# Optimization experiments

Hardware: AMD Instinct MI355X
Metric: run time of the kernel (lower is better)

Reference implementation:

```python
import jax, jax.numpy as jnp
import numpy as np

N = 100000      # nodes
E = 1250000     # edges
D = 64          # hidden_units == dim_node_features
DE = 7          # edge feature dim (OGBG-PPA)
L = 5           # num_layers
G = 128         # graphs in batch
T = 37          # classes


def setup_inputs() -> dict:
    key = jax.random.key(0)
    ks = jax.random.split(key, 12)
    x = jax.random.normal(ks[0], (N, D), dtype=jnp.float32)
    edge_index = jax.random.randint(ks[1], (2, E), 0, N, dtype=jnp.int64)
    edge_attr = jax.random.uniform(ks[2], (E, DE), dtype=jnp.float32)
    batch = jnp.sort(jax.random.randint(ks[3], (N,), 0, G, dtype=jnp.int64))
    s_e = 1.0 / np.sqrt(DE)
    s_d = 1.0 / np.sqrt(D)
    s_p = 1.0 / np.sqrt(L * D)
    W_edge = jax.random.normal(ks[4], (DE, D), dtype=jnp.float32) * s_e  # shared edge encoder
    b_edge = jnp.zeros((D,), jnp.float32)
    W_mlp = jax.random.normal(ks[5], (L, D, D), dtype=jnp.float32) * s_d  # per-layer MLP
    b_mlp = jnp.zeros((L, D), jnp.float32)
    eps = jnp.zeros((L,), jnp.float32)  # torch.Tensor([0]) per layer
    W_pred = jax.random.normal(ks[6], (L * D, T), dtype=jnp.float32) * s_p
    b_pred = jnp.zeros((T,), jnp.float32)
    return {"x": x, "edge_index": edge_index, "edge_attr": edge_attr, "batch": batch,
            "W_edge": W_edge, "b_edge": b_edge, "eps": eps,
            "W_mlp": W_mlp, "b_mlp": b_mlp, "W_pred": W_pred, "b_pred": b_pred}


def reference(x, edge_index, edge_attr, batch, W_edge, b_edge, eps, W_mlp, b_mlp, W_pred, b_pred):
    src, dst = edge_index[0], edge_index[1]  # PyG source_to_target: x_j = x[src], aggregate at dst
    # shared edge encoder -> identical output every layer; compute once
    edge_emb = edge_attr @ W_edge + b_edge  # [E, D]
    h = x
    outs = []
    for i in range(L):
        msg = jax.nn.relu(h[src] + edge_emb)                      # gather + fuse  [E, D]
        agg = jax.ops.segment_sum(msg, dst, num_segments=N)       # scatter-add    [N, D]
        h = jax.nn.relu(((1.0 + eps[i]) * h + agg) @ W_mlp[i] + b_mlp[i])
        outs.append(h)
    node_emb = jnp.concatenate(outs, axis=1)                      # [N, L*D]
    # predictor: per-graph mean pool + linear readout
    g_sum = jax.ops.segment_sum(node_emb, batch, num_segments=G)  # [G, L*D]
    cnt = jax.ops.segment_sum(jnp.ones((N, 1), node_emb.dtype), batch, num_segments=G)
    g = g_sum / jnp.maximum(cnt, 1.0)
    return g @ W_pred + b_pred                                    # [G, T]
```

## Files before the change

### kernel.cpp

```cpp
#include <hip/hip_runtime.h>
#include <hip/hip_bf16.h>

#define DD   64
#define NL   5
#define NT   37
#define LD   (NL*DD)
#define PB   16
#define NBMAX 512

typedef __attribute__((ext_vector_type(8))) short short8;
typedef __attribute__((ext_vector_type(4))) float f32x4;
typedef __attribute__((ext_vector_type(4))) int   i32x4;
typedef __attribute__((ext_vector_type(2))) int   i32x2;

static __device__ __forceinline__ int padq(int d) { return (d + PB - 1) & ~(PB - 1); }
static __device__ __forceinline__ short bf16_bits(float f) {
    __hip_bfloat16 h = __float2bfloat16(f);
    return __builtin_bit_cast(short, h);
}
static __device__ __forceinline__ float bf2f(short s) {
    return __int_as_float(((int)(unsigned short)s) << 16);
}

__global__ void init_kernel(const float* __restrict__ x, __hip_bfloat16* __restrict__ hb,
                            size_t n1, const float* __restrict__ W,
                            __hip_bfloat16* __restrict__ Wt, int n2,
                            const int* __restrict__ dst, int* __restrict__ deg, int E,
                            int do_deg) {
    size_t i = (size_t)blockIdx.x * blockDim.x + threadIdx.x;
    if (i < n1) {
        hb[i] = __float2bfloat16(x[i]);
    } else if (i < n1 + (size_t)n2) {
        size_t id = i - n1;
        int l = (int)(id / (DD * DD));
        int r = (int)(id % (DD * DD));
        int c = r / DD, k = r % DD;
        Wt[(size_t)l * DD * DD + c * DD + k] =
            __float2bfloat16(W[(size_t)l * DD * DD + k * DD + c]);
    } else if (do_deg) {
        size_t e = i - n1 - (size_t)n2;
        if (e < (size_t)E) atomicAdd(&deg[dst[e]], 1);
    }
}

__global__ void bhist_kernel(const int* __restrict__ dst, int* __restrict__ bcnt, int E) {
    __shared__ int h[NBMAX];
    int tid = threadIdx.x;
    h[tid] = 0; h[tid + 256] = 0;
    __syncthreads();
    int base = blockIdx.x * 4096;
#pragma unroll
    for (int j = 0; j < 16; ++j) {
        int e = base + j * 256 + tid;
        if (e < E) atomicAdd(&h[dst[e] >> 8], 1);
    }
    __syncthreads();
    int c0 = h[tid], c1 = h[tid + 256];
    if (c0) atomicAdd(&bcnt[tid], c0);
    if (c1) atomicAdd(&bcnt[tid + 256], c1);
}

__global__ void bscan_kernel(const int* __restrict__ bcnt, int* __restrict__ boff,
                             int* __restrict__ bcur) {
    __shared__ int sm[256];
    int tid = threadIdx.x;
    int v0 = bcnt[2 * tid], v1 = bcnt[2 * tid + 1];
    int s = v0 + v1;
    sm[tid] = s;
    __syncthreads();
    for (int off = 1; off < 256; off <<= 1) {
        int t = (tid >= off) ? sm[tid - off] : 0;
        __syncthreads();
        sm[tid] += t;
        __syncthreads();
    }
    int p = sm[tid] - s;
    boff[2 * tid] = p;     bcur[2 * tid] = p;     p += v0;
    boff[2 * tid + 1] = p; bcur[2 * tid + 1] = p; p += v1;
    if (tid == 255) boff[512] = p;
}

__global__ void pscat_kernel(const int* __restrict__ dst, int* __restrict__ bcur,
                             i32x2* __restrict__ stage, int E) {
    __shared__ int h[NBMAX];
    __shared__ int runb[NBMAX];
    int tid = threadIdx.x;
    h[tid] = 0; h[tid + 256] = 0;
    __syncthreads();
    int base = blockIdx.x * 4096;
    int d[16];
#pragma unroll
    for (int j = 0; j < 16; ++j) {
        int e = base + j * 256 + tid;
        d[j] = (e < E) ? dst[e] : -1;
        if (d[j] >= 0) atomicAdd(&h[d[j] >> 8], 1);
    }
    __syncthreads();
    int c0 = h[tid], c1 = h[tid + 256];
    runb[tid]       = c0 ? atomicAdd(&bcur[tid], c0) : 0;
    runb[tid + 256] = c1 ? atomicAdd(&bcur[tid + 256], c1) : 0;
    __syncthreads();
    h[tid] = 0; h[tid + 256] = 0;
    __syncthreads();
#pragma unroll
    for (int j = 0; j < 16; ++j) {
        if (d[j] >= 0) {
            int b = d[j] >> 8;
            int r = atomicAdd(&h[b], 1);
            i32x2 pr; pr[0] = base + j * 256 + tid; pr[1] = d[j];
            stage[runb[b] + r] = pr;
        }
    }
}

__global__ void bdeg_kernel(const i32x2* __restrict__ stage, const int* __restrict__ boff,
                            int* __restrict__ deg, int n) {
    __shared__ int cnt[256];
    int tid = threadIdx.x;
    int b = blockIdx.x;
    cnt[tid] = 0;
    __syncthreads();
    int s = boff[b], e = boff[b + 1];
    for (int j = s + tid; j < e; j += 256)
        atomicAdd(&cnt[stage[j][1] & 255], 1);
    __syncthreads();
    int node = b * 256 + tid;
    if (node < n) deg[node] = cnt[tid];
}

template<bool PACKED>
__global__ void place_kernel(const i32x2* __restrict__ stage, const int* __restrict__ boff,
                             const int* __restrict__ rowptr, const int* __restrict__ src,
                             const float* __restrict__ ea,
                             short* __restrict__ eab, int* __restrict__ srcv,
                             int* __restrict__ col, int n) {
    __shared__ int cur[256];
    int tid = threadIdx.x;
    int b = blockIdx.x;
    int node = b * 256 + tid;
    cur[tid] = (node < n) ? rowptr[node] : 0;
    __syncthreads();
    int s = boff[b], e = boff[b + 1];
    for (int j = s + tid; j < e; j += 256) {
        i32x2 pr = stage[j];
        int eid = pr[0], d = pr[1];
        int slot = atomicAdd(&cur[d & 255], 1);
        srcv[slot] = src[eid];
        if (PACKED) {
            const float* a = ea + (size_t)eid * 7;
            short8 r;
#pragma unroll
            for (int k = 0; k < 7; ++k) r[k] = bf16_bits(a[k]);
            r[7] = 0;
            *((i32x4*)(eab + (size_t)slot * 8)) = __builtin_bit_cast(i32x4, r);
        } else {
            col[slot] = eid;
        }
    }
    __syncthreads();
    if (node < n) {
        int endp = rowptr[node + 1];
        for (int i = cur[tid]; i < endp; ++i) {
            srcv[i] = 0;
            if (PACKED) {
                i32x4 z = {0, 0, 0, 0};
                *((i32x4*)(eab + (size_t)i * 8)) = z;
            } else {
                col[i] = 0;
            }
        }
    }
}

__global__ void chunksum_kernel(const int* __restrict__ deg, int* __restrict__ csum, int n) {
    __shared__ int sm[256];
    int tid = threadIdx.x;
    int base = blockIdx.x * 1024 + tid * 4;
    int s = 0;
#pragma unroll
    for (int j = 0; j < 4; ++j) s += (base + j < n) ? padq(deg[base + j]) : 0;
    sm[tid] = s;
    __syncthreads();
    for (int off = 128; off > 0; off >>= 1) {
        if (tid < off) sm[tid] += sm[tid + off];
        __syncthreads();
    }
    if (tid == 0) csum[blockIdx.x] = sm[0];
}

__global__ void scansums_kernel(int* __restrict__ csum, int nc, int* __restrict__ tot) {
    __shared__ int sm[256];
    int tid = threadIdx.x;
    int base = tid * 4;
    int v[4]; int s = 0;
#pragma unroll
    for (int j = 0; j < 4; ++j) { v[j] = (base + j < nc) ? csum[base + j] : 0; s += v[j]; }
    sm[tid] = s;
    __syncthreads();
    for (int off = 1; off < 256; off <<= 1) {
        int t = (tid >= off) ? sm[tid - off] : 0;
        __syncthreads();
        sm[tid] += t;
        __syncthreads();
    }
    int p = sm[tid] - s;
#pragma unroll
    for (int j = 0; j < 4; ++j) { if (base + j < nc) csum[base + j] = p; p += v[j]; }
    if (tid == 255) *tot = p;
}

__global__ void chunkscan_kernel(const int* __restrict__ deg, const int* __restrict__ csum,
                                 int* __restrict__ rowptr, int* __restrict__ cursor, int n) {
    __shared__ int sm[256];
    int tid = threadIdx.x;
    int base = blockIdx.x * 1024 + tid * 4;
    int v[4]; int s = 0;
#pragma unroll
    for (int j = 0; j < 4; ++j) { v[j] = (base + j < n) ? padq(deg[base + j]) : 0; s += v[j]; }
    sm[tid] = s;
    __syncthreads();
    for (int off = 1; off < 256; off <<= 1) {
        int t = (tid >= off) ? sm[tid - off] : 0;
        __syncthreads();
        sm[tid] += t;
        __syncthreads();
    }
    int p = sm[tid] - s + csum[blockIdx.x];
#pragma unroll
    for (int j = 0; j < 4; ++j) {
        if (base + j < n) { rowptr[base + j] = p; cursor[base + j] = p; }
        p += v[j];
    }
}

__global__ void fillpos_kernel(const int* __restrict__ dst, int* __restrict__ cursor,
                               int* __restrict__ col, int E) {
    int e = blockIdx.x * blockDim.x + threadIdx.x;
    if (e >= E) return;
    int p = atomicAdd(&cursor[dst[e]], 1);
    col[p] = e;
}

__global__ void padmark_kernel(const int* __restrict__ deg, const int* __restrict__ rowptr,
                               int* __restrict__ col, int n) {
    int v = blockIdx.x * blockDim.x + threadIdx.x;
    if (v >= n) return;
    int s = rowptr[v] + deg[v];
    int e = rowptr[v + 1];
    for (int i = s; i < e; ++i) col[i] = -1;
}

template<bool PACKED>
__global__ void gfill_kernel(const int* __restrict__ col, const int* __restrict__ src,
                             const float* __restrict__ ea, const int* __restrict__ rowptrN,
                             short* __restrict__ eab, int* __restrict__ srcv,
                             int* __restrict__ colw) {
    int slot = blockIdx.x * blockDim.x + threadIdx.x;
    if (slot >= *rowptrN) return;
    int e = col[slot];
    int s = 0;
    short8 r;
#pragma unroll
    for (int k = 0; k < 8; ++k) r[k] = 0;
    if (e >= 0) {
        s = src[e];
        if (PACKED) {
            const float* a = ea + (size_t)e * 7;
#pragma unroll
            for (int k = 0; k < 7; ++k) r[k] = bf16_bits(a[k]);
        }
    } else if (!PACKED) {
        colw[slot] = 0;
    }
    __builtin_nontemporal_store(s, &srcv[slot]);
    if (PACKED) {
        i32x4 ri = __builtin_bit_cast(i32x4, r);
        __builtin_nontemporal_store(ri, (i32x4*)(eab + (size_t)slot * 8));
    }
}

template<bool PACKED>
__global__ void fill_kernel(const int* __restrict__ dst, const int* __restrict__ src,
                            const float* __restrict__ ea, int* __restrict__ cursor,
                            short* __restrict__ eab, int* __restrict__ col,
                            int* __restrict__ srcv, int E) {
    int e = blockIdx.x * blockDim.x + threadIdx.x;
    if (e >= E) return;
    int p = atomicAdd(&cursor[dst[e]], 1);
    int s = src[e];
    __builtin_nontemporal_store(s, &srcv[p]);
    if (PACKED) {
        const float* a = ea + (size_t)e * 7;
        short8 r;
#pragma unroll
        for (int k = 0; k < 7; ++k) r[k] = bf16_bits(a[k]);
        r[7] = 0;
        i32x4 ri = __builtin_bit_cast(i32x4, r);
        __builtin_nontemporal_store(ri, (i32x4*)(eab + (size_t)p * 8));
    } else {
        __builtin_nontemporal_store(e, &col[p]);
    }
}

__global__ void padfill_kernel(const int* __restrict__ deg, const int* __restrict__ rowptr,
                               int* __restrict__ srcv, int* __restrict__ col,
                               int has_col, int n) {
    int v = blockIdx.x * blockDim.x + threadIdx.x;
    if (v >= n) return;
    int s = rowptr[v] + deg[v];
    int e = rowptr[v + 1];
    for (int i = s; i < e; ++i) {
        srcv[i] = 0;
        if (has_col) col[i] = 0;
    }
}

template<bool PACKED>
static __device__ __forceinline__ float row_partial(
    const __hip_bfloat16* __restrict__ hb_in, const short* __restrict__ eab,
    const int* __restrict__ col, const float* __restrict__ ea,
    const int* __restrict__ srcv, int beg, int dv, int lane,
    const float* __restrict__ we, float be) {
    float acc = 0.f;
    int end = beg + dv;
    for (int p = beg; p < end; p += PB) {
        int mm = end - p;
        int S[PB];
#pragma unroll
        for (int j = 0; j < PB; ++j) S[j] = srcv[p + j];
        __hip_bfloat16 hv[PB];
#pragma unroll
        for (int j = 0; j < PB; ++j) hv[j] = hb_in[(size_t)S[j] * DD + lane];
        float ev[PB][7];
        if (PACKED) {
            short8 eb[PB];
#pragma unroll
            for (int j = 0; j < PB; ++j)
                eb[j] = *((const short8*)(eab + (size_t)(p + j) * 8));
#pragma unroll
            for (int j = 0; j < PB; ++j)
#pragma unroll
                for (int k = 0; k < 7; ++k) ev[j][k] = bf2f(eb[j][k]);
        } else {
            int EJ[PB];
#pragma unroll
            for (int j = 0; j < PB; ++j) EJ[j] = col[p + j];
#pragma unroll
            for (int j = 0; j < PB; ++j) {
                const float* a = ea + (size_t)EJ[j] * 7;
#pragma unroll
                for (int k = 0; k < 7; ++k) ev[j][k] = a[k];
            }
        }
#pragma unroll
        for (int j = 0; j < PB; ++j) {
            if (j < mm) {
                float emb = be + ev[j][0] * we[0] + ev[j][1] * we[1] + ev[j][2] * we[2]
                               + ev[j][3] * we[3] + ev[j][4] * we[4] + ev[j][5] * we[5]
                               + ev[j][6] * we[6];
                float tv = __bfloat162float(hv[j]) + emb;
                acc += (tv > 0.f) ? tv : 0.f;
            }
        }
    }
    return acc;
}

template<bool PACKED>
static __device__ __forceinline__ void agg_pair(
    const __hip_bfloat16* __restrict__ hb_in, const short* __restrict__ eab,
    const int* __restrict__ col, const float* __restrict__ ea,
    const int* __restrict__ srcv, int beg0, int d0, int beg1, int d1, bool has1,
    int lane, const float* __restrict__ we, float be, float& acc0, float& acc1) {
    acc0 = 0.f; acc1 = 0.f;
    if (has1 && d0 >= 1 && d0 <= PB && d1 >= 1 && d1 <= PB) {
        int S0[PB], S1[PB];
#pragma unroll
        for (int j = 0; j < PB; ++j) S0[j] = srcv[beg0 + j];
#pragma unroll
        for (int j = 0; j < PB; ++j) S1[j] = srcv[beg1 + j];
        __hip_bfloat16 hv0[PB], hv1[PB];
#pragma unroll
        for (int j = 0; j < PB; ++j) hv0[j] = hb_in[(size_t)S0[j] * DD + lane];
#pragma unroll
        for (int j = 0; j < PB; ++j) hv1[j] = hb_in[(size_t)S1[j] * DD + lane];
        float ev0[PB][7], ev1[PB][7];
        if (PACKED) {
            short8 eb0[PB], eb1[PB];
#pragma unroll
            for (int j = 0; j < PB; ++j)
                eb0[j] = *((const short8*)(eab + (size_t)(beg0 + j) * 8));
#pragma unroll
            for (int j = 0; j < PB; ++j)
                eb1[j] = *((const short8*)(eab + (size_t)(beg1 + j) * 8));
#pragma unroll
            for (int j = 0; j < PB; ++j)
#pragma unroll
                for (int k = 0; k < 7; ++k) ev0[j][k] = bf2f(eb0[j][k]);
#pragma unroll
            for (int j = 0; j < PB; ++j)
#pragma unroll
                for (int k = 0; k < 7; ++k) ev1[j][k] = bf2f(eb1[j][k]);
        } else {
            int EJ0[PB], EJ1[PB];
#pragma unroll
            for (int j = 0; j < PB; ++j) EJ0[j] = col[beg0 + j];
#pragma unroll
            for (int j = 0; j < PB; ++j) EJ1[j] = col[beg1 + j];
#pragma unroll
            for (int j = 0; j < PB; ++j) {
                const float* a = ea + (size_t)EJ0[j] * 7;
#pragma unroll
                for (int k = 0; k < 7; ++k) ev0[j][k] = a[k];
            }
#pragma unroll
            for (int j = 0; j < PB; ++j) {
                const float* a = ea + (size_t)EJ1[j] * 7;
#pragma unroll
                for (int k = 0; k < 7; ++k) ev1[j][k] = a[k];
            }
        }
#pragma unroll
        for (int j = 0; j < PB; ++j) {
            if (j < d0) {
                float emb = be + ev0[j][0] * we[0] + ev0[j][1] * we[1] + ev0[j][2] * we[2]
                               + ev0[j][3] * we[3] + ev0[j][4] * we[4] + ev0[j][5] * we[5]
                               + ev0[j][6] * we[6];
                float tv = __bfloat162float(hv0[j]) + emb;
                acc0 += (tv > 0.f) ? tv : 0.f;
            }
        }
#pragma unroll
        for (int j = 0; j < PB; ++j) {
            if (j < d1) {
                float emb = be + ev1[j][0] * we[0] + ev1[j][1] * we[1] + ev1[j][2] * we[2]
                               + ev1[j][3] * we[3] + ev1[j][4] * we[4] + ev1[j][5] * we[5]
                               + ev1[j][6] * we[6];
                float tv = __bfloat162float(hv1[j]) + emb;
                acc1 += (tv > 0.f) ? tv : 0.f;
            }
        }
    } else {
        acc0 = row_partial<PACKED>(hb_in, eab, col, ea, srcv, beg0, d0, lane, we, be);
        if (has1)
            acc1 = row_partial<PACKED>(hb_in, eab, col, ea, srcv, beg1, d1, lane, we, be);
    }
}

__global__ __launch_bounds__(256, 4)
void aggmlp_kernel(const __hip_bfloat16* __restrict__ hb_in,
                   const short* __restrict__ eab, const int* __restrict__ srcv,
                   const int* __restrict__ rowptr, const int* __restrict__ deg,
                   const float* __restrict__ W_edge, const float* __restrict__ b_edge,
                   const float* __restrict__ eps, int layer,
                   const __hip_bfloat16* __restrict__ Wt, const float* __restrict__ bmlp,
                   __hip_bfloat16* __restrict__ hb_out, int n) {
    __shared__ __align__(16) short uls[16][72];
    int tid = threadIdx.x;
    int lane = tid & 63;
    int wv = __builtin_amdgcn_readfirstlane(tid >> 6);
    int base = blockIdx.x * 16;

    float we[7];
#pragma unroll
    for (int k = 0; k < 7; ++k) we[k] = W_edge[k * DD + lane];
    float be = b_edge[lane];
    float epsv = 1.f + eps[layer];

#pragma unroll
    for (int pp = 0; pp < 2; ++pp) {
        int v0 = base + wv * 4 + pp * 2;
        bool h0 = v0 < n, h1 = (v0 + 1) < n;
        int beg0 = h0 ? rowptr[v0] : 0;
        int d0   = h0 ? deg[v0] : 0;
        int beg1 = h1 ? rowptr[v0 + 1] : 0;
        int d1   = h1 ? deg[v0 + 1] : 0;
        float acc0, acc1;
        agg_pair<true>(hb_in, eab, nullptr, nullptr, srcv,
                       beg0, d0, beg1, d1, h1, lane, we, be, acc0, acc1);
        if (h0) {
            float self = __bfloat162float(hb_in[(size_t)v0 * DD + lane]);
            uls[wv * 4 + pp * 2][lane] = bf16_bits(epsv * self + acc0);
        }
        if (h1) {
            float self = __bfloat162float(hb_in[(size_t)(v0 + 1) * DD + lane]);
            uls[wv * 4 + pp * 2 + 1][lane] = bf16_bits(epsv * self + acc1);
        }
    }
    __syncthreads();

    if (wv == 0) {
        int colx = lane & 15;
        int quad = lane >> 4;
        short8 wf[4][2];
#pragma unroll
        for (int t = 0; t < 4; ++t)
#pragma unroll
            for (int s = 0; s < 2; ++s)
                wf[t][s] = *((const short8*)(Wt + (size_t)(t * 16 + colx) * DD + s * 32 + quad * 8));
        float bias[4];
#pragma unroll
        for (int t = 0; t < 4; ++t) bias[t] = bmlp[t * 16 + colx];

        short8 a0 = *((const short8*)&uls[colx][quad * 8]);
        short8 a1 = *((const short8*)&uls[colx][32 + quad * 8]);

        f32x4 acc[4] = {{0.f, 0.f, 0.f, 0.f}, {0.f, 0.f, 0.f, 0.f},
                        {0.f, 0.f, 0.f, 0.f}, {0.f, 0.f, 0.f, 0.f}};
#pragma unroll
        for (int t = 0; t < 4; ++t) {
            acc[t] = __builtin_amdgcn_mfma_f32_16x16x32_bf16(a0, wf[t][0], acc[t], 0, 0, 0);
            acc[t] = __builtin_amdgcn_mfma_f32_16x16x32_bf16(a1, wf[t][1], acc[t], 0, 0, 0);
        }
#pragma unroll
        for (int r = 0; r < 4; ++r) {
            int v = base + quad * 4 + r;
            if (v < n) {
#pragma unroll
                for (int t = 0; t < 4; ++t) {
                    float val = acc[t][r] + bias[t];
                    val = (val > 0.f) ? val : 0.f;
                    hb_out[(size_t)v * DD + t * 16 + colx] = __float2bfloat16(val);
                }
            }
        }
    }
}

template<bool PACKED>
__global__ __launch_bounds__(256, 4)
void agg_kernel(const __hip_bfloat16* __restrict__ hb_in,
                const short* __restrict__ eab,
                const int* __restrict__ col, const int* __restrict__ srcv,
                const float* __restrict__ ea,
                const int* __restrict__ rowptr, const int* __restrict__ deg,
                const float* __restrict__ W_edge, const float* __restrict__ b_edge,
                const float* __restrict__ eps, int layer,
                __hip_bfloat16* __restrict__ u, int n) {
    int lane = threadIdx.x & 63;
    int wid = __builtin_amdgcn_readfirstlane(blockIdx.x * 4 + (threadIdx.x >> 6));
    int v0 = wid * 2;
    if (v0 >= n) return;

    float we[7];
#pragma unroll
    for (int k = 0; k < 7; ++k) we[k] = W_edge[k * DD + lane];
    float be = b_edge[lane];
    float epsv = 1.f + eps[layer];

    int beg0 = rowptr[v0];
    int d0   = deg[v0];
    bool has1 = (v0 + 1) < n;
    int beg1 = has1 ? rowptr[v0 + 1] : 0;
    int d1   = has1 ? deg[v0 + 1] : 0;

    float acc0, acc1;
    agg_pair<PACKED>(hb_in, eab, col, ea, srcv, beg0, d0, beg1, d1, has1,
                     lane, we, be, acc0, acc1);

    float self0 = __bfloat162float(hb_in[(size_t)v0 * DD + lane]);
    u[(size_t)v0 * DD + lane] = __float2bfloat16(epsv * self0 + acc0);
    if (has1) {
        float self1 = __bfloat162float(hb_in[(size_t)(v0 + 1) * DD + lane]);
        u[(size_t)(v0 + 1) * DD + lane] = __float2bfloat16(epsv * self1 + acc1);
    }
}

__global__ __launch_bounds__(256, 4)
void mlp_mfma_kernel(const __hip_bfloat16* __restrict__ u,
                     const __hip_bfloat16* __restrict__ Wt,
                     const float* __restrict__ bmlp,
                     __hip_bfloat16* __restrict__ hb_out, int n) {
    int lane = threadIdx.x & 63;
    int wid  = threadIdx.x >> 6;
    int colx = lane & 15;
    int quad = lane >> 4;
    int v0 = __builtin_amdgcn_readfirstlane((blockIdx.x * 4 + wid) * 16);
    if (v0 >= n) return;

    short8 wf[4][2];
#pragma unroll
    for (int t = 0; t < 4; ++t)
#pragma unroll
        for (int s = 0; s < 2; ++s)
            wf[t][s] = *((const short8*)(Wt + (size_t)(t * 16 + colx) * DD + s * 32 + quad * 8));
    float bias[4];
#pragma unroll
    for (int t = 0; t < 4; ++t) bias[t] = bmlp[t * 16 + colx];

    int vr = v0 + colx;
    int vrc = (vr < n) ? vr : (n - 1);
    const __hip_bfloat16* up = u + (size_t)vrc * DD;
    short8 a0 = *((const short8*)(up + quad * 8));
    short8 a1 = *((const short8*)(up + 32 + quad * 8));

    f32x4 acc[4] = {{0.f, 0.f, 0.f, 0.f}, {0.f, 0.f, 0.f, 0.f},
                    {0.f, 0.f, 0.f, 0.f}, {0.f, 0.f, 0.f, 0.f}};
#pragma unroll
    for (int t = 0; t < 4; ++t) {
        acc[t] = __builtin_amdgcn_mfma_f32_16x16x32_bf16(a0, wf[t][0], acc[t], 0, 0, 0);
        acc[t] = __builtin_amdgcn_mfma_f32_16x16x32_bf16(a1, wf[t][1], acc[t], 0, 0, 0);
    }

#pragma unroll
    for (int r = 0; r < 4; ++r) {
        int v = v0 + quad * 4 + r;
        if (v < n) {
#pragma unroll
            for (int t = 0; t < 4; ++t) {
                float val = acc[t][r] + bias[t];
                val = (val > 0.f) ? val : 0.f;
                hb_out[(size_t)v * DD + t * 16 + colx] = __float2bfloat16(val);
            }
        }
    }
}

__global__ void pool_part_kernel(const __hip_bfloat16* __restrict__ htabs, size_t lstride,
                                 const int* __restrict__ batch,
                                 float* __restrict__ g_sum, int n, int G) {
    __shared__ float part[4][DD];
    __shared__ int bnd[2];
    int g = blockIdx.x / NL;
    int q = blockIdx.x % NL;
    int tid = threadIdx.x;
    if (tid < 2) {
        int target = g + tid;
        int lo = 0, hi = n;
        while (lo < hi) { int mid = (lo + hi) >> 1; if (batch[mid] < target) lo = mid + 1; else hi = mid; }
        bnd[tid] = lo;
    }
    __syncthreads();
    int lb = bnd[0], ub = bnd[1];
    int w = tid >> 6, f = tid & 63;
    const __hip_bfloat16* T = htabs + (size_t)q * lstride;
    float s = 0.f;
    for (int v = lb + w; v < ub; v += 4)
        s += __bfloat162float(T[(size_t)v * DD + f]);
    part[w][f] = s;
    __syncthreads();
    if (tid < DD) {
        float tot = part[0][f] + part[1][f] + part[2][f] + part[3][f];
        float c = (float)(ub - lb);
        if (c < 1.f) c = 1.f;
        g_sum[(size_t)g * LD + q * DD + f] = tot / c;
    }
}

__global__ void readout_mean_kernel(const float* __restrict__ g_mean,
                                    const float* __restrict__ W_pred,
                                    const float* __restrict__ b_pred,
                                    float* __restrict__ out, int G) {
    int id = blockIdx.x * blockDim.x + threadIdx.x;
    if (id >= G * NT) return;
    int g = id / NT, t = id % NT;
    float acc = b_pred[t];
    const float* gs = g_mean + (size_t)g * LD;
    for (int k = 0; k < LD; ++k) acc += gs[k] * W_pred[k * NT + t];
    out[id] = acc;
}

__global__ void pool_kernel(const __hip_bfloat16* __restrict__ h, const int* __restrict__ batch,
                            float* __restrict__ g_sum, int layer, int n) {
    int wave = (blockIdx.x * blockDim.x + threadIdx.x) >> 6;
    int l = threadIdx.x & 63;
    int v0 = wave * 64;
    if (v0 >= n) return;
    int vend = min(v0 + 64, n);
    int cur = batch[v0];
    float acc = 0.f;
    for (int v = v0; v < vend; ++v) {
        int bv = batch[v];
        if (bv != cur) {
            atomicAdd(&g_sum[(size_t)cur * LD + layer * DD + l], acc);
            acc = 0.f;
            cur = bv;
        }
        acc += __bfloat162float(h[(size_t)v * DD + l]);
    }
    atomicAdd(&g_sum[(size_t)cur * LD + layer * DD + l], acc);
}

__global__ void graph_cnt_kernel(const int* __restrict__ batch, int* __restrict__ cnt,
                                 int n, int G) {
    int g = blockIdx.x * blockDim.x + threadIdx.x;
    if (g >= G) return;
    int lo = 0, hi = n;
    while (lo < hi) { int mid = (lo + hi) >> 1; if (batch[mid] < g) lo = mid + 1; else hi = mid; }
    int lb0 = lo;
    lo = lb0; hi = n;
    while (lo < hi) { int mid = (lo + hi) >> 1; if (batch[mid] < g + 1) lo = mid + 1; else hi = mid; }
    cnt[g] = lo - lb0;
}

__global__ void readout_kernel(const float* __restrict__ g_sum, const int* __restrict__ cnt,
                               const float* __restrict__ W_pred, const float* __restrict__ b_pred,
                               float* __restrict__ out, int G) {
    int id = blockIdx.x * blockDim.x + threadIdx.x;
    if (id >= G * NT) return;
    int g = id / NT, t = id % NT;
    float c = (float)cnt[g];
    if (c < 1.f) c = 1.f;
    float inv = 1.f / c;
    float acc = b_pred[t];
    const float* gs = g_sum + (size_t)g * LD;
    for (int k = 0; k < LD; ++k) acc += gs[k] * inv * W_pred[k * NT + t];
    out[id] = acc;
}

extern "C" void kernel_launch(void* const* d_in, const int* in_sizes, int n_in,
                              void* d_out, int out_size, void* d_ws, size_t ws_size,
                              hipStream_t stream) {
    const float* x       = (const float*)d_in[0];
    const int*   eidx    = (const int*)d_in[1];
    const float* ea      = (const float*)d_in[2];
    const int*   batch   = (const int*)d_in[3];
    const float* W_edge  = (const float*)d_in[4];
    const float* b_edge  = (const float*)d_in[5];
    const float* eps     = (const float*)d_in[6];
    const float* W_mlp   = (const float*)d_in[7];
    const float* b_mlp   = (const float*)d_in[8];
    const float* W_pred  = (const float*)d_in[9];
    const float* b_pred  = (const float*)d_in[10];
    float* out = (float*)d_out;

    const int N = in_sizes[3];
    const int E = in_sizes[2] / 7;
    const int G = out_size / NT;
    const int* src = eidx;
    const int* dst = eidx + E;
    const int NC = (N + 1023) / 1024;
    const int NB = (N + 255) >> 8;
    const size_t SLOTS = (size_t)E + (size_t)(PB - 1) * N;

    const size_t S_h = (size_t)N * DD * 2;
    const size_t small = (size_t)N * 4 + (size_t)(N + 4) * 4 + (size_t)N * 4 + 4096
                       + 8192
                       + (size_t)NL * DD * DD * 2
                       + (size_t)G * LD * 4 + (((size_t)G * 4 + 15) & ~(size_t)15);
    const size_t needA = 7 * S_h + small + SLOTS * 20;
    const size_t needB = 7 * S_h + small + SLOTS * 8;
    const int tier = (ws_size >= needA) ? 0 : (ws_size >= needB) ? 1 : 2;
    const int nTab = (tier <= 1) ? 6 : 2;

    char* w = (char*)d_ws;
    __hip_bfloat16* hbt = (__hip_bfloat16*)w;  w += (size_t)nTab * S_h;
    __hip_bfloat16* u   = (__hip_bfloat16*)w;  w += S_h;
    __hip_bfloat16* Wt  = (__hip_bfloat16*)w;  w += (size_t)NL * DD * DD * 2;
    int*   deg    = (int*)w;                   w += (size_t)N * 4;
    int*   rowptr = (int*)w;                   w += (size_t)(N + 4) * 4;
    int*   cursor = (int*)w;                   w += (size_t)N * 4;
    int*   csum   = (int*)w;                   w += 4096;
    int*   bcnt   = (int*)w;                   w += 2048;
    int*   boff   = (int*)w;                   w += 2064;
    int*   bcur   = (int*)w;                   w += 2048;
    float* g_sum  = (float*)w;                 w += (size_t)G * LD * 4;
    int*   cnt    = (int*)w;                   w += ((size_t)G * 4 + 15) & ~(size_t)15;
    short* eab = nullptr; int* col = nullptr; int* srcv = nullptr;
    if (tier == 0) {
        eab  = (short*)w;  w += SLOTS * 16;
        srcv = (int*)w;
    } else {
        col  = (int*)w;    w += SLOTS * 4;
        srcv = (int*)w;
    }
    const bool packed = (tier == 0);

    const bool newcsr = (NB <= NBMAX) && ((size_t)E * 8 <= S_h);
    i32x2* stage = (i32x2*)u;

    if (tier == 2) hipMemsetAsync(g_sum, 0, (size_t)G * LD * 4, stream);

    {
        size_t n1 = (size_t)N * DD;
        size_t tot = n1 + (size_t)(NL * DD * DD) + (newcsr ? 0 : (size_t)E);
        if (!newcsr) hipMemsetAsync(deg, 0, (size_t)N * 4, stream);
        init_kernel<<<(unsigned)((tot + 255) / 256), 256, 0, stream>>>(
            x, hbt, n1, W_mlp, Wt, NL * DD * DD, dst, deg, E, newcsr ? 0 : 1);
    }

    if (newcsr) {
        hipMemsetAsync(bcnt, 0, NBMAX * 4, stream);
        unsigned eb4 = (unsigned)((E + 4095) / 4096);
        bhist_kernel<<<eb4, 256, 0, stream>>>(dst, bcnt, E);
        bscan_kernel<<<1, 256, 0, stream>>>(bcnt, boff, bcur);
        pscat_kernel<<<eb4, 256, 0, stream>>>(dst, bcur, stage, E);
        bdeg_kernel<<<NB, 256, 0, stream>>>(stage, boff, deg, N);
        chunksum_kernel<<<NC, 256, 0, stream>>>(deg, csum, N);
        scansums_kernel<<<1, 256, 0, stream>>>(csum, NC, rowptr + N);
        chunkscan_kernel<<<NC, 256, 0, stream>>>(deg, csum, rowptr, cursor, N);
        if (packed)
            place_kernel<true><<<NB, 256, 0, stream>>>(stage, boff, rowptr, src, ea,
                                                       eab, srcv, col, N);
        else
            place_kernel<false><<<NB, 256, 0, stream>>>(stage, boff, rowptr, src, ea,
                                                        eab, srcv, col, N);
    } else {
        chunksum_kernel<<<NC, 256, 0, stream>>>(deg, csum, N);
        scansums_kernel<<<1, 256, 0, stream>>>(csum, NC, rowptr + N);
        chunkscan_kernel<<<NC, 256, 0, stream>>>(deg, csum, rowptr, cursor, N);
        int* colbuf = nullptr;
        if (tier == 0) {
            if (SLOTS * 4 <= S_h) colbuf = (int*)u;
        } else {
            colbuf = col;
        }
        if (colbuf) {
            fillpos_kernel<<<(E + 255) / 256, 256, 0, stream>>>(dst, cursor, colbuf, E);
            padmark_kernel<<<(N + 255) / 256, 256, 0, stream>>>(deg, rowptr, colbuf, N);
            unsigned gblocks = (unsigned)((SLOTS + 255) / 256);
            if (packed)
                gfill_kernel<true><<<gblocks, 256, 0, stream>>>(colbuf, src, ea, rowptr + N,
                                                                eab, srcv, colbuf);
            else
                gfill_kernel<false><<<gblocks, 256, 0, stream>>>(colbuf, src, ea, rowptr + N,
                                                                 eab, srcv, colbuf);
        } else {
            if (packed)
                fill_kernel<true><<<(E + 255) / 256, 256, 0, stream>>>(dst, src, ea, cursor,
                                                                       eab, col, srcv, E);
            else
                fill_kernel<false><<<(E + 255) / 256, 256, 0, stream>>>(dst, src, ea, cursor,
                                                                        eab, col, srcv, E);
            padfill_kernel<<<(N + 255) / 256, 256, 0, stream>>>(deg, rowptr, srcv,
                                                                col ? col : srcv,
                                                                col ? 1 : 0, N);
        }
    }

    const bool useFused = newcsr && packed;
    int fusedBlocks = (N + 15) / 16;
    int aggBlocks = (N + 7) / 8;
    int mlpBlocks = (N + 63) / 64;
    for (int i = 0; i < NL; ++i) {
        __hip_bfloat16* hin  = (tier <= 1) ? (hbt + (size_t)i * N * DD)
                                           : (hbt + (size_t)(i & 1) * N * DD);
        __hip_bfloat16* hout = (tier <= 1) ? (hbt + (size_t)(i + 1) * N * DD)
                                           : (hbt + (size_t)((i + 1) & 1) * N * DD);
        if (useFused) {
            aggmlp_kernel<<<fusedBlocks, 256, 0, stream>>>(
                hin, eab, srcv, rowptr, deg, W_edge, b_edge, eps, i,
                Wt + (size_t)i * DD * DD, b_mlp + (size_t)i * DD, hout, N);
        } else {
            if (packed)
                agg_kernel<true><<<aggBlocks, 256, 0, stream>>>(
                    hin, eab, col, srcv, ea, rowptr, deg, W_edge, b_edge, eps, i, u, N);
            else
                agg_kernel<false><<<aggBlocks, 256, 0, stream>>>(
                    hin, eab, col, srcv, ea, rowptr, deg, W_edge, b_edge, eps, i, u, N);
            mlp_mfma_kernel<<<mlpBlocks, 256, 0, stream>>>(
                u, Wt + (size_t)i * DD * DD, b_mlp + (size_t)i * DD, hout, N);
        }
        if (tier == 2)
            pool_kernel<<<((N + 63) / 64 * 64 + 255) / 256, 256, 0, stream>>>(hout, batch,
                                                                              g_sum, i, N);
    }

    if (tier <= 1) {
        pool_part_kernel<<<G * NL, 256, 0, stream>>>(hbt + (size_t)N * DD, (size_t)N * DD,
                                                     batch, g_sum, N, G);
        readout_mean_kernel<<<(G * NT + 255) / 256, 256, 0, stream>>>(g_sum, W_pred, b_pred,
                                                                      out, G);
    } else {
        graph_cnt_kernel<<<1, 128, 0, stream>>>(batch, cnt, N, G);
        readout_kernel<<<(G * NT + 255) / 256, 256, 0, stream>>>(g_sum, cnt, W_pred, b_pred,
                                                                 out, G);
    }
}
```

Before: 674.6 us.

## Compute edge embeddings with MFMA in fused aggregate-MLP kernel

The fused aggregation kernel now computes the per-edge encoder projection with a bf16 16x16x32 MFMA. It packs edge features with a constant 1.0 in the 8th slot so the bias folds into a padded transposed weight table, built in init_kernel. Each wave processes one node at a time: lanes split into four edge groups and 16 feature columns, then reduce with cross-lane shuffles. This replaces the scalar 7-term FMA per edge per feature. The bcnt memset is folded into init_kernel to save a launch, and the paired-node path is removed, which may reduce memory-level parallelism for gathers.

```diff
diff --git a/kernel.cpp b/kernel.cpp
--- a/kernel.cpp
+++ b/kernel.cpp
@@ -25,6 +25,8 @@
 __global__ void init_kernel(const float* __restrict__ x, __hip_bfloat16* __restrict__ hb,
                             size_t n1, const float* __restrict__ W,
                             __hip_bfloat16* __restrict__ Wt, int n2,
+                            const float* __restrict__ W_edge, const float* __restrict__ b_edge,
+                            __hip_bfloat16* __restrict__ webt, int* __restrict__ bcnt,
                             const int* __restrict__ dst, int* __restrict__ deg, int E,
                             int do_deg) {
     size_t i = (size_t)blockIdx.x * blockDim.x + threadIdx.x;
@@ -37,8 +39,15 @@
         int c = r / DD, k = r % DD;
         Wt[(size_t)l * DD * DD + c * DD + k] =
             __float2bfloat16(W[(size_t)l * DD * DD + k * DD + c]);
+    } else if (i < n1 + (size_t)n2 + 2048) {
+        int id = (int)(i - n1 - (size_t)n2);
+        int f = id >> 5, k = id & 31;
+        float v = (k < 7) ? W_edge[k * DD + f] : (k == 7 ? b_edge[f] : 0.f);
+        webt[id] = __float2bfloat16(v);
+    } else if (i < n1 + (size_t)n2 + 2048 + NBMAX) {
+        bcnt[i - n1 - (size_t)n2 - 2048] = 0;
     } else if (do_deg) {
-        size_t e = i - n1 - (size_t)n2;
+        size_t e = i - n1 - (size_t)n2 - 2048 - NBMAX;
         if (e < (size_t)E) atomicAdd(&deg[dst[e]], 1);
     }
 }
@@ -151,7 +160,7 @@
             short8 r;
 #pragma unroll
             for (int k = 0; k < 7; ++k) r[k] = bf16_bits(a[k]);
-            r[7] = 0;
+            r[7] = (short)0x3F80;
             *((i32x4*)(eab + (size_t)slot * 8)) = __builtin_bit_cast(i32x4, r);
         } else {
             col[slot] = eid;
@@ -268,6 +277,7 @@
             const float* a = ea + (size_t)e * 7;
 #pragma unroll
             for (int k = 0; k < 7; ++k) r[k] = bf16_bits(a[k]);
+            r[7] = (short)0x3F80;
         }
     } else if (!PACKED) {
         colw[slot] = 0;
@@ -294,7 +304,7 @@
         short8 r;
 #pragma unroll
         for (int k = 0; k < 7; ++k) r[k] = bf16_bits(a[k]);
-        r[7] = 0;
+        r[7] = (short)0x3F80;
         i32x4 ri = __builtin_bit_cast(i32x4, r);
         __builtin_nontemporal_store(ri, (i32x4*)(eab + (size_t)p * 8));
     } else {
@@ -372,79 +382,10 @@
     const int* __restrict__ col, const float* __restrict__ ea,
     const int* __restrict__ srcv, int beg0, int d0, int beg1, int d1, bool has1,
     int lane, const float* __restrict__ we, float be, float& acc0, float& acc1) {
-    acc0 = 0.f; acc1 = 0.f;
-    if (has1 && d0 >= 1 && d0 <= PB && d1 >= 1 && d1 <= PB) {
-        int S0[PB], S1[PB];
-#pragma unroll
-        for (int j = 0; j < PB; ++j) S0[j] = srcv[beg0 + j];
-#pragma unroll
-        for (int j = 0; j < PB; ++j) S1[j] = srcv[beg1 + j];
-        __hip_bfloat16 hv0[PB], hv1[PB];
-#pragma unroll
-        for (int j = 0; j < PB; ++j) hv0[j] = hb_in[(size_t)S0[j] * DD + lane];
-#pragma unroll
-        for (int j = 0; j < PB; ++j) hv1[j] = hb_in[(size_t)S1[j] * DD + lane];
-        float ev0[PB][7], ev1[PB][7];
-        if (PACKED) {
-            short8 eb0[PB], eb1[PB];
-#pragma unroll
-            for (int j = 0; j < PB; ++j)
-                eb0[j] = *((const short8*)(eab + (size_t)(beg0 + j) * 8));
-#pragma unroll
-            for (int j = 0; j < PB; ++j)
-                eb1[j] = *((const short8*)(eab + (size_t)(beg1 + j) * 8));
-#pragma unroll
-            for (int j = 0; j < PB; ++j)
-#pragma unroll
-                for (int k = 0; k < 7; ++k) ev0[j][k] = bf2f(eb0[j][k]);
-#pragma unroll
-            for (int j = 0; j < PB; ++j)
-#pragma unroll
-                for (int k = 0; k < 7; ++k) ev1[j][k] = bf2f(eb1[j][k]);
-        } else {
-            int EJ0[PB], EJ1[PB];
-#pragma unroll
-            for (int j = 0; j < PB; ++j) EJ0[j] = col[beg0 + j];
-#pragma unroll
-            for (int j = 0; j < PB; ++j) EJ1[j] = col[beg1 + j];
-#pragma unroll
-            for (int j = 0; j < PB; ++j) {
-                const float* a = ea + (size_t)EJ0[j] * 7;
-#pragma unroll
-                for (int k = 0; k < 7; ++k) ev0[j][k] = a[k];
-            }
-#pragma unroll
-            for (int j = 0; j < PB; ++j) {
-                const float* a = ea + (size_t)EJ1[j] * 7;
-#pragma unroll
-                for (int k = 0; k < 7; ++k) ev1[j][k] = a[k];
-            }
-        }
-#pragma unroll
-        for (int j = 0; j < PB; ++j) {
-            if (j < d0) {
-                float emb = be + ev0[j][0] * we[0] + ev0[j][1] * we[1] + ev0[j][2] * we[2]
-                               + ev0[j][3] * we[3] + ev0[j][4] * we[4] + ev0[j][5] * we[5]
-                               + ev0[j][6] * we[6];
-                float tv = __bfloat162float(hv0[j]) + emb;
-                acc0 += (tv > 0.f) ? tv : 0.f;
-            }
-        }
-#pragma unroll
-        for (int j = 0; j < PB; ++j) {
-            if (j < d1) {
-                float emb = be + ev1[j][0] * we[0] + ev1[j][1] * we[1] + ev1[j][2] * we[2]
-                               + ev1[j][3] * we[3] + ev1[j][4] * we[4] + ev1[j][5] * we[5]
-                               + ev1[j][6] * we[6];
-                float tv = __bfloat162float(hv1[j]) + emb;
-                acc1 += (tv > 0.f) ? tv : 0.f;
-            }
-        }
-    } else {
-        acc0 = row_partial<PACKED>(hb_in, eab, col, ea, srcv, beg0, d0, lane, we, be);
-        if (has1)
-            acc1 = row_partial<PACKED>(hb_in, eab, col, ea, srcv, beg1, d1, lane, we, be);
-    }
+    acc0 = row_partial<PACKED>(hb_in, eab, col, ea, srcv, beg0, d0, lane, we, be);
+    acc1 = 0.f;
+    if (has1)
+        acc1 = row_partial<PACKED>(hb_in, eab, col, ea, srcv, beg1, d1, lane, we, be);
 }
 
 __global__ __launch_bounds__(256, 4)
@@ -452,14 +393,18 @@
                    const short* __restrict__ eab, const int* __restrict__ srcv,
                    const int* __restrict__ rowptr, const int* __restrict__ deg,
                    const float* __restrict__ W_edge, const float* __restrict__ b_edge,
+                   const __hip_bfloat16* __restrict__ webt,
                    const float* __restrict__ eps, int layer,
                    const __hip_bfloat16* __restrict__ Wt, const float* __restrict__ bmlp,
                    __hip_bfloat16* __restrict__ hb_out, int n) {
     __shared__ __align__(16) short uls[16][72];
+    const unsigned short* hbu = (const unsigned short*)hb_in;
     int tid = threadIdx.x;
     int lane = tid & 63;
     int wv = __builtin_amdgcn_readfirstlane(tid >> 6);
     int base = blockIdx.x * 16;
+    int colx = lane & 15;
+    int q = lane >> 4;
 
     float we[7];
 #pragma unroll
@@ -467,43 +412,77 @@
     float be = b_edge[lane];
     float epsv = 1.f + eps[layer];
 
-#pragma unroll
-    for (int pp = 0; pp < 2; ++pp) {
-        int v0 = base + wv * 4 + pp * 2;
-        bool h0 = v0 < n, h1 = (v0 + 1) < n;
-        int beg0 = h0 ? rowptr[v0] : 0;
-        int d0   = h0 ? deg[v0] : 0;
-        int beg1 = h1 ? rowptr[v0 + 1] : 0;
-        int d1   = h1 ? deg[v0 + 1] : 0;
-        float acc0, acc1;
-        agg_pair<true>(hb_in, eab, nullptr, nullptr, srcv,
-                       beg0, d0, beg1, d1, h1, lane, we, be, acc0, acc1);
-        if (h0) {
-            float self = __bfloat162float(hb_in[(size_t)v0 * DD + lane]);
-            uls[wv * 4 + pp * 2][lane] = bf16_bits(epsv * self + acc0);
-        }
-        if (h1) {
-            float self = __bfloat162float(hb_in[(size_t)(v0 + 1) * DD + lane]);
-            uls[wv * 4 + pp * 2 + 1][lane] = bf16_bits(epsv * self + acc1);
+    short8 wb[4];
+#pragma unroll
+    for (int t = 0; t < 4; ++t)
+        wb[t] = *((const short8*)(webt + (size_t)(t * 16 + colx) * 32 + q * 8));
+
+#pragma unroll
+    for (int nd = 0; nd < 4; ++nd) {
+        int v = base + wv * 4 + nd;
+        if (v < n) {
+            int p = rowptr[v];
+            int d = deg[v];
+            float nodeacc;
+            if (d >= 1 && d <= PB) {
+                short8 a = {0, 0, 0, 0, 0, 0, 0, 0};
+                if (q == 0)
+                    a = *((const short8*)(eab + (size_t)(p + colx) * 8));
+                int sr0 = srcv[p + 4 * q + 0];
+                int sr1 = srcv[p + 4 * q + 1];
+                int sr2 = srcv[p + 4 * q + 2];
+                int sr3 = srcv[p + 4 * q + 3];
+                f32x4 z = {0.f, 0.f, 0.f, 0.f};
+                f32x4 emb[4];
+#pragma unroll
+                for (int t = 0; t < 4; ++t)
+                    emb[t] = __builtin_amdgcn_mfma_f32_16x16x32_bf16(a, wb[t], z, 0, 0, 0);
+                unsigned short hv[4][4];
+#pragma unroll
+                for (int t = 0; t < 4; ++t) {
+                    hv[0][t] = hbu[(size_t)sr0 * DD + t * 16 + colx];
+                    hv[1][t] = hbu[(size_t)sr1 * DD + t * 16 + colx];
+                    hv[2][t] = hbu[(size_t)sr2 * DD + t * 16 + colx];
+                    hv[3][t] = hbu[(size_t)sr3 * DD + t * 16 + colx];
+                }
+                float ts[4];
+#pragma unroll
+                for (int t = 0; t < 4; ++t) {
+                    float s = 0.f;
+#pragma unroll
+                    for (int r = 0; r < 4; ++r) {
+                        float tv = __int_as_float((int)hv[r][t] << 16) + emb[t][r];
+                        float rv = ((4 * q + r) < d) ? ((tv > 0.f) ? tv : 0.f) : 0.f;
+                        s += rv;
+                    }
+                    s += __shfl_xor(s, 16, 64);
+                    s += __shfl_xor(s, 32, 64);
+                    ts[t] = s;
+                }
+                nodeacc = (q == 0) ? ts[0] : (q == 1) ? ts[1] : (q == 2) ? ts[2] : ts[3];
+            } else {
+                nodeacc = row_partial<true>(hb_in, eab, nullptr, nullptr, srcv,
+                                            p, d, lane, we, be);
+            }
+            float self = __int_as_float((int)hbu[(size_t)v * DD + lane] << 16);
+            uls[wv * 4 + nd][lane] = bf16_bits(epsv * self + nodeacc);
         }
     }
     __syncthreads();
 
     if (wv == 0) {
-        int colx = lane & 15;
-        int quad = lane >> 4;
         short8 wf[4][2];
 #pragma unroll
         for (int t = 0; t < 4; ++t)
 #pragma unroll
             for (int s = 0; s < 2; ++s)
-                wf[t][s] = *((const short8*)(Wt + (size_t)(t * 16 + colx) * DD + s * 32 + quad * 8));
+                wf[t][s] = *((const short8*)(Wt + (size_t)(t * 16 + colx) * DD + s * 32 + q * 8));
         float bias[4];
 #pragma unroll
         for (int t = 0; t < 4; ++t) bias[t] = bmlp[t * 16 + colx];
 
-        short8 a0 = *((const short8*)&uls[colx][quad * 8]);
-        short8 a1 = *((const short8*)&uls[colx][32 + quad * 8]);
+        short8 a0 = *((const short8*)&uls[colx][q * 8]);
+        short8 a1 = *((const short8*)&uls[colx][32 + q * 8]);
 
         f32x4 acc[4] = {{0.f, 0.f, 0.f, 0.f}, {0.f, 0.f, 0.f, 0.f},
                         {0.f, 0.f, 0.f, 0.f}, {0.f, 0.f, 0.f, 0.f}};
@@ -514,7 +493,7 @@
         }
 #pragma unroll
         for (int r = 0; r < 4; ++r) {
-            int v = base + quad * 4 + r;
+            int v = base + q * 4 + r;
             if (v < n) {
 #pragma unroll
                 for (int t = 0; t < 4; ++t) {
@@ -735,7 +714,7 @@
 
     const size_t S_h = (size_t)N * DD * 2;
     const size_t small = (size_t)N * 4 + (size_t)(N + 4) * 4 + (size_t)N * 4 + 4096
-                       + 8192
+                       + 8192 + 4096
                        + (size_t)NL * DD * DD * 2
                        + (size_t)G * LD * 4 + (((size_t)G * 4 + 15) & ~(size_t)15);
     const size_t needA = 7 * S_h + small + SLOTS * 20;
@@ -747,6 +726,7 @@
     __hip_bfloat16* hbt = (__hip_bfloat16*)w;  w += (size_t)nTab * S_h;
     __hip_bfloat16* u   = (__hip_bfloat16*)w;  w += S_h;
     __hip_bfloat16* Wt  = (__hip_bfloat16*)w;  w += (size_t)NL * DD * DD * 2;
+    __hip_bfloat16* webt = (__hip_bfloat16*)w; w += 4096;
     int*   deg    = (int*)w;                   w += (size_t)N * 4;
     int*   rowptr = (int*)w;                   w += (size_t)(N + 4) * 4;
     int*   cursor = (int*)w;                   w += (size_t)N * 4;
@@ -773,14 +753,14 @@
 
     {
         size_t n1 = (size_t)N * DD;
-        size_t tot = n1 + (size_t)(NL * DD * DD) + (newcsr ? 0 : (size_t)E);
+        size_t tot = n1 + (size_t)(NL * DD * DD) + 2048 + NBMAX + (newcsr ? 0 : (size_t)E);
         if (!newcsr) hipMemsetAsync(deg, 0, (size_t)N * 4, stream);
         init_kernel<<<(unsigned)((tot + 255) / 256), 256, 0, stream>>>(
-            x, hbt, n1, W_mlp, Wt, NL * DD * DD, dst, deg, E, newcsr ? 0 : 1);
+            x, hbt, n1, W_mlp, Wt, NL * DD * DD, W_edge, b_edge, webt, bcnt,
+            dst, deg, E, newcsr ? 0 : 1);
     }
 
     if (newcsr) {
-        hipMemsetAsync(bcnt, 0, NBMAX * 4, stream);
         unsigned eb4 = (unsigned)((E + 4095) / 4096);
         bhist_kernel<<<eb4, 256, 0, stream>>>(dst, bcnt, E);
         bscan_kernel<<<1, 256, 0, stream>>>(bcnt, boff, bcur);
@@ -839,7 +819,7 @@
                                            : (hbt + (size_t)((i + 1) & 1) * N * DD);
         if (useFused) {
             aggmlp_kernel<<<fusedBlocks, 256, 0, stream>>>(
-                hin, eab, srcv, rowptr, deg, W_edge, b_edge, eps, i,
+                hin, eab, srcv, rowptr, deg, W_edge, b_edge, webt, eps, i,
                 Wt + (size_t)i * DD * DD, b_mlp + (size_t)i * DD, hout, N);
         } else {
             if (packed)
```

Result: faster. 600.8 us (-10.9%).
